# Kernel tuning notes

Hardware: AMD Instinct MI355X
Metric: run time of the kernel (lower is better)

## Reference

```python
import jax, jax.numpy as jnp
import numpy as np
import math

B, S, D, H = 2, 2048, 1024, 16
HD = D // H  # head_dim = 64

def setup_inputs() -> dict:
    key = jax.random.key(0)
    ks = jax.random.split(key, 11)
    def n(k, shape, scale=1.0):
        return jax.random.normal(k, shape, dtype=jnp.float32) * scale
    w_scale = 1.0 / math.sqrt(D)
    return {
        "q": n(ks[0], (B, S, D)),
        "k": n(ks[1], (B, S, D)),
        "v": n(ks[2], (B, S, D)),
        "WQ_w": n(ks[3], (D, D), w_scale),
        "WQ_b": n(ks[4], (D,), 0.01),
        "WK_w": n(ks[5], (D, D), w_scale),
        "WK_b": n(ks[6], (D,), 0.01),
        "WV_w": n(ks[7], (D, D), w_scale),
        "WV_b": n(ks[8], (D,), 0.01),
        "Wout_w": n(ks[9], (D, D), w_scale),
        "Wout_b": n(ks[10], (D,), 0.01),
    }

def reference(q, k, v, WQ_w, WQ_b, WK_w, WK_b, WV_w, WV_b, Wout_w, Wout_b):
    b, s, _ = k.shape
    # QKV projections (torch Linear: x @ W.T + b; here weights stored [in, out])
    qh = (q @ WQ_w + WQ_b).reshape(b, -1, H, HD).transpose(0, 2, 1, 3)  # [b,h,s,hd]
    kh = (k @ WK_w + WK_b).reshape(b, -1, H, HD).transpose(0, 2, 1, 3)
    vh = (v @ WV_w + WV_b).reshape(b, -1, H, HD).transpose(0, 2, 1, 3)
    # naive attention: full [b,h,s,s] score matrix
    scores = jnp.einsum("bhqd,bhkd->bhqk", qh, kh) / math.sqrt(HD)
    attn = jax.nn.softmax(scores, axis=-1)
    out = jnp.einsum("bhqk,bhkd->bhqd", attn, vh)
    concat = out.transpose(0, 2, 1, 3).reshape(b, -1, H * HD)  # [b,s,inner_dim]
    return concat @ Wout_w + Wout_b
```

## Files before the change

### kernel.cpp

```cpp
#include <hip/hip_runtime.h>
#include <hip/hip_bf16.h>
#include <stdint.h>

typedef __attribute__((ext_vector_type(8))) short bf16x8;
typedef __attribute__((ext_vector_type(4))) short short4v;
typedef __attribute__((ext_vector_type(4))) float f32x4;

#define MFMA16x16x32 __builtin_amdgcn_mfma_f32_16x16x32_bf16

__device__ __forceinline__ short f2b(float f) {
  union { float f; uint32_t u; } x;
  x.f = f;
  uint32_t u = x.u;
  uint32_t r = (u + 0x7FFFu + ((u >> 16) & 1u)) >> 16;
  return (short)(uint16_t)r;
}

__device__ __forceinline__ uint32_t cvt_pk_bf16(float lo, float hi) {
  uint32_t r;
  asm volatile("v_cvt_pk_bf16_f32 %0, %1, %2" : "=v"(r) : "v"(lo), "v"(hi));
  return r;
}
__device__ __forceinline__ float exp2_fast(float x) {
  float r;
  asm volatile("v_exp_f32 %0, %1" : "=v"(r) : "v"(x));
  return r;
}
__device__ __forceinline__ bf16x8 cvt8(const float4 a, const float4 b) {
  union { uint32_t u[4]; bf16x8 v; } o;
  o.u[0] = cvt_pk_bf16(a.x, a.y);
  o.u[1] = cvt_pk_bf16(a.z, a.w);
  o.u[2] = cvt_pk_bf16(b.x, b.y);
  o.u[3] = cvt_pk_bf16(b.z, b.w);
  return o.v;
}

__device__ __forceinline__ void async_copy16(const void* g, void* l) {
  __builtin_amdgcn_global_load_lds(
      (const __attribute__((address_space(1))) void*)g,
      (__attribute__((address_space(3))) void*)l, 16, 0, 0);
}

__global__ void prep_kernel(const float* __restrict__ W0,
                            const float* __restrict__ W1,
                            const float* __restrict__ W2,
                            const float* __restrict__ W3,
                            const float* __restrict__ q,
                            const float* __restrict__ k,
                            const float* __restrict__ v,
                            short* __restrict__ Wt,
                            short* __restrict__ xq,
                            short* __restrict__ xk,
                            short* __restrict__ xv) {
  __shared__ short tile[64][72];
  const int z = blockIdx.z;
  const int t = threadIdx.x;
  if (z < 4) {
    const float* W = (z == 0) ? W0 : (z == 1) ? W1 : (z == 2) ? W2 : W3;
    short* Wo = Wt + (size_t)z * 1024 * 1024;
    const int r0 = blockIdx.y * 64;
    const int c0 = blockIdx.x * 64;
#pragma unroll
    for (int i = 0; i < 4; ++i) {
      const int lin = i * 1024 + t * 4;
      const int r = lin >> 6, c = lin & 63;
      const float4 vv = *(const float4*)&W[(size_t)(r0 + r) * 1024 + c0 + c];
      tile[r][c + 0] = f2b(vv.x);
      tile[r][c + 1] = f2b(vv.y);
      tile[r][c + 2] = f2b(vv.z);
      tile[r][c + 3] = f2b(vv.w);
    }
    __syncthreads();
#pragma unroll
    for (int i = 0; i < 2; ++i) {
      const int lin = i * 2048 + t * 8;
      const int r = lin >> 6, c = lin & 63;
      bf16x8 ov;
#pragma unroll
      for (int jj = 0; jj < 8; ++jj) ov[jj] = tile[c + jj][r];
      *(bf16x8*)&Wo[(size_t)(c0 + r) * 1024 + r0 + c] = ov;
    }
  } else {
    const float* x = (z == 4) ? q : (z == 5) ? k : v;
    short* yp = (z == 4) ? xq : (z == 5) ? xk : xv;
    const int base = (blockIdx.y * 16 + blockIdx.x) * 256 + t;
#pragma unroll
    for (int j = 0; j < 8; ++j) {
      const int i = base + j * 65536;
      const float4 a = ((const float4*)x)[2 * i];
      const float4 b = ((const float4*)x)[2 * i + 1];
      ((bf16x8*)yp)[i] = cvt8(a, b);
    }
  }
}

__launch_bounds__(256, 2)
__global__ void gemm_qkv_kernel(const short* __restrict__ A0,
                                const short* __restrict__ A1,
                                const short* __restrict__ A2,
                                const short* __restrict__ WtBase,
                                const float* __restrict__ b0,
                                const float* __restrict__ b1,
                                const float* __restrict__ b2,
                                short* __restrict__ C0,
                                short* __restrict__ C1,
                                short* __restrict__ Vt,
                                int ybase) {
  const int K = 1024;
  __shared__ short As[128 * 64];
  __shared__ short Bs[128 * 64];

  const int y = blockIdx.y + ybase;
  const short* A = (y == 0) ? A0 : (y == 1) ? A1 : A2;
  const short* Wt = WtBase + (size_t)y * 1024 * 1024;
  const float* bias = (y == 0) ? b0 : (y == 1) ? b1 : b2;

  const int tm = blockIdx.x & 31;
  const int tn = blockIdx.x >> 5;
  const int m0 = tm * 128, n0 = tn * 128;

  const int tid = threadIdx.x;
  const int lane = tid & 63;
  const int w = tid >> 6;
  const int wr = w >> 1, wc = w & 1;
  const int hi = lane >> 4, cc = lane & 15;
  const int srow = lane >> 3, schunk = lane & 7;

  f32x4 acc[4][4] = {};

  for (int kt = 0; kt < 16; ++kt) {
    const int k0 = kt * 64;
#pragma unroll
    for (int i = 0; i < 4; ++i) {
      const int ri = w * 4 + i;
      const int row = ri * 8 + srow;
      const int gch = schunk ^ (row & 7);
      async_copy16(A + (size_t)(m0 + row) * K + (k0 + gch * 8), &As[ri * 512]);
      async_copy16(Wt + (size_t)(n0 + row) * K + (k0 + gch * 8), &Bs[ri * 512]);
    }
    __syncthreads();
#pragma unroll
    for (int kk = 0; kk < 2; ++kk) {
      bf16x8 af[4], bfr[4];
#pragma unroll
      for (int x = 0; x < 4; ++x) {
        const int gch = kk * 4 + hi;
        const int rowA = wr * 64 + x * 16 + cc;
        af[x] = *(const bf16x8*)&As[rowA * 64 + ((gch ^ (rowA & 7)) << 3)];
        const int rowB = wc * 64 + x * 16 + cc;
        bfr[x] = *(const bf16x8*)&Bs[rowB * 64 + ((gch ^ (rowB & 7)) << 3)];
      }
#pragma unroll
      for (int x = 0; x < 4; ++x)
#pragma unroll
        for (int yy = 0; yy < 4; ++yy)
          acc[x][yy] = MFMA16x16x32(af[x], bfr[yy], acc[x][yy], 0, 0, 0);
    }
    __syncthreads();
  }

  short* Cout = (y == 0) ? C0 : C1;
#pragma unroll
  for (int x = 0; x < 4; ++x) {
    const int rbase = m0 + wr * 64 + x * 16 + (hi << 2);
#pragma unroll
    for (int yy = 0; yy < 4; ++yy) {
      const int col = n0 + wc * 64 + yy * 16 + cc;
      const float bv = bias[col];
      if (y == 2) {
        const int b = rbase >> 11, s = rbase & 2047;
        const int hh = col >> 6, d = col & 63;
        short4v pack;
#pragma unroll
        for (int r = 0; r < 4; ++r) pack[r] = f2b(acc[x][yy][r] + bv);
        *(short4v*)&Vt[((size_t)(b * 16 + hh) * 64 + d) * 2048 + s] = pack;
      } else {
#pragma unroll
        for (int r = 0; r < 4; ++r)
          Cout[(size_t)(rbase + r) * 1024 + col] = f2b(acc[x][yy][r] + bv);
      }
    }
  }
}

__launch_bounds__(256, 2)
__global__ void gemm_out_kernel(const short* __restrict__ A,
                                const short* __restrict__ Wt,
                                const float* __restrict__ bias,
                                float* __restrict__ C) {
  const int N = 1024, K = 1024;
  __shared__ short As[128 * 64];
  __shared__ short Bs[128 * 64];

  const int tm = blockIdx.x & 31;
  const int tn = blockIdx.x >> 5;
  const int m0 = tm * 128, n0 = tn * 128;

  const int tid = threadIdx.x;
  const int lane = tid & 63;
  const int w = tid >> 6;
  const int wr = w >> 1, wc = w & 1;
  const int hi = lane >> 4, cc = lane & 15;
  const int srow = lane >> 3, schunk = lane & 7;

  f32x4 acc[4][4] = {};

  for (int kt = 0; kt < 16; ++kt) {
    const int k0 = kt * 64;
#pragma unroll
    for (int i = 0; i < 4; ++i) {
      const int ri = w * 4 + i;
      const int row = ri * 8 + srow;
      const int gch = schunk ^ (row & 7);
      async_copy16(A + (size_t)(m0 + row) * K + (k0 + gch * 8), &As[ri * 512]);
      async_copy16(Wt + (size_t)(n0 + row) * K + (k0 + gch * 8), &Bs[ri * 512]);
    }
    __syncthreads();
#pragma unroll
    for (int kk = 0; kk < 2; ++kk) {
      bf16x8 af[4], bfr[4];
#pragma unroll
      for (int x = 0; x < 4; ++x) {
        const int gch = kk * 4 + hi;
        const int rowA = wr * 64 + x * 16 + cc;
        af[x] = *(const bf16x8*)&As[rowA * 64 + ((gch ^ (rowA & 7)) << 3)];
        const int rowB = wc * 64 + x * 16 + cc;
        bfr[x] = *(const bf16x8*)&Bs[rowB * 64 + ((gch ^ (rowB & 7)) << 3)];
      }
#pragma unroll
      for (int x = 0; x < 4; ++x)
#pragma unroll
        for (int yy = 0; yy < 4; ++yy)
          acc[x][yy] = MFMA16x16x32(af[x], bfr[yy], acc[x][yy], 0, 0, 0);
    }
    __syncthreads();
  }

#pragma unroll
  for (int x = 0; x < 4; ++x) {
    const int rbase = m0 + wr * 64 + x * 16 + (hi << 2);
#pragma unroll
    for (int yy = 0; yy < 4; ++yy) {
      const int col = n0 + wc * 64 + yy * 16 + cc;
      const float bv = bias[col];
#pragma unroll
      for (int r = 0; r < 4; ++r)
        C[(size_t)(rbase + r) * N + col] = acc[x][yy][r] + bv;
    }
  }
}

__launch_bounds__(256, 2)
__global__ void attn_kernel(const short* __restrict__ qh,
                            const short* __restrict__ kh,
                            const short* __restrict__ Vt,
                            short* __restrict__ concat) {
  const float CL2 = 0.18033688011112042f;
  __shared__ short Ks[2][64 * 64];
  __shared__ short Vs[2][64 * 64];

  const int qb = blockIdx.x;
  const int h = blockIdx.y;
  const int b = blockIdx.z;
  const int tid = threadIdx.x, lane = tid & 63, w = tid >> 6;
  const int hi = lane >> 4, cc = lane & 15;

  const size_t rowbase = (size_t)b * 2048;
  const int q0 = qb * 128 + w * 32;

  bf16x8 qf[2][2];
#pragma unroll
  for (int aq = 0; aq < 2; ++aq)
#pragma unroll
    for (int kk = 0; kk < 2; ++kk) {
      const int col = h * 64 + kk * 32 + hi * 8;
      qf[aq][kk] =
          *(const bf16x8*)&qh[(rowbase + q0 + aq * 16 + cc) * 1024 + col];
    }

  f32x4 oacc[2][4] = {};
  float l[2] = {0.f, 0.f};
  bf16x8 vf[2][4];
  uint32_t pu[2][4][2];

  const short* Vth = Vt + (size_t)(b * 16 + h) * 64 * 2048;
  const int srow = lane >> 3, schunk = lane & 7;
  const int fKr = (((cc >> 2) & 1) << 2) | (cc & 3);

  auto STAGE = [&](int tile, int buf) {
#pragma unroll
    for (int i = 0; i < 2; ++i) {
      const int ri = w * 2 + i;
      const int row = ri * 8 + srow;
      const int gchK = schunk ^ ((((ri) & 1) << 2) | (srow & 3));
      const int gchV = schunk ^ (row & 7);
      async_copy16(&kh[(rowbase + tile * 64 + row) * 1024 + h * 64 + gchK * 8],
                   &Ks[buf][ri * 512]);
      async_copy16(&Vth[(size_t)row * 2048 + tile * 64 + gchV * 8],
                   &Vs[buf][ri * 512]);
    }
  };
  auto QK = [&](int buf, f32x4 (&sacc)[2][4]) {
#pragma unroll
    for (int kk = 0; kk < 2; ++kk) {
      bf16x8 kf[4];
#pragma unroll
      for (int n = 0; n < 4; ++n) {
        const int row = ((n >> 1) << 5) + (((cc >> 2)) << 3) + ((n & 1) << 2) +
                        (cc & 3);
        const int ch = (kk * 4 + hi) ^ fKr;
        kf[n] = *(const bf16x8*)&Ks[buf][row * 64 + (ch << 3)];
      }
#pragma unroll
      for (int aq = 0; aq < 2; ++aq)
#pragma unroll
        for (int n = 0; n < 4; ++n)
          sacc[aq][n] = MFMA16x16x32(kf[n], qf[aq][kk], sacc[aq][n], 0, 0, 0);
    }
  };
  auto LOADV = [&](int buf) {
#pragma unroll
    for (int kvh = 0; kvh < 2; ++kvh) {
      const int ch = (kvh * 4 + hi) ^ (cc & 7);
#pragma unroll
      for (int n = 0; n < 4; ++n)
        vf[kvh][n] =
            *(const bf16x8*)&Vs[buf][(n * 16 + cc) * 64 + (ch << 3)];
    }
  };
  auto SOFTMAX = [&](f32x4 (&sacc)[2][4]) {
#pragma unroll
    for (int aq = 0; aq < 2; ++aq)
#pragma unroll
      for (int n = 0; n < 4; ++n) {
        const float p0 = exp2_fast(sacc[aq][n][0] * CL2);
        const float p1 = exp2_fast(sacc[aq][n][1] * CL2);
        const float p2 = exp2_fast(sacc[aq][n][2] * CL2);
        const float p3 = exp2_fast(sacc[aq][n][3] * CL2);
        l[aq] += (p0 + p1) + (p2 + p3);
        pu[aq][n][0] = cvt_pk_bf16(p0, p1);
        pu[aq][n][1] = cvt_pk_bf16(p2, p3);
      }
  };
  auto PV = [&]() {
#pragma unroll
    for (int kvh = 0; kvh < 2; ++kvh)
#pragma unroll
      for (int aq = 0; aq < 2; ++aq) {
        union { uint32_t u[4]; bf16x8 v; } pf;
        pf.u[0] = pu[aq][2 * kvh][0];
        pf.u[1] = pu[aq][2 * kvh][1];
        pf.u[2] = pu[aq][2 * kvh + 1][0];
        pf.u[3] = pu[aq][2 * kvh + 1][1];
#pragma unroll
        for (int n = 0; n < 4; ++n)
          oacc[aq][n] = MFMA16x16x32(vf[kvh][n], pf.v, oacc[aq][n], 0, 0, 0);
      }
  };

  STAGE(0, 0);
  __syncthreads();
  {
    STAGE(1, 1);
    f32x4 sacc[2][4] = {};
    QK(0, sacc);
    LOADV(0);
    SOFTMAX(sacc);
    __syncthreads();
  }

  for (int t = 1; t < 32; ++t) {
    const int cur = t & 1;
    if (t + 1 < 32) STAGE(t + 1, cur ^ 1);
    f32x4 sacc[2][4] = {};
    QK(cur, sacc);
    PV();
    LOADV(cur);
    SOFTMAX(sacc);
    __syncthreads();
  }
  PV();

#pragma unroll
  for (int aq = 0; aq < 2; ++aq) {
    float lv = l[aq];
    lv += __shfl_xor(lv, 16);
    lv += __shfl_xor(lv, 32);
    const float inv = 1.0f / lv;
    const size_t grow = rowbase + q0 + aq * 16 + cc;
#pragma unroll
    for (int n = 0; n < 4; ++n)
#pragma unroll
      for (int r = 0; r < 4; ++r) {
        const int d = n * 16 + hi * 4 + r;
        concat[grow * 1024 + h * 64 + d] = f2b(oacc[aq][n][r] * inv);
      }
  }
}

extern "C" void kernel_launch(void* const* d_in, const int* in_sizes, int n_in,
                              void* d_out, int out_size, void* d_ws, size_t ws_size,
                              hipStream_t stream) {
  const float* q = (const float*)d_in[0];
  const float* k = (const float*)d_in[1];
  const float* v = (const float*)d_in[2];
  const float* WQ = (const float*)d_in[3];
  const float* bQ = (const float*)d_in[4];
  const float* WK = (const float*)d_in[5];
  const float* bK = (const float*)d_in[6];
  const float* WV = (const float*)d_in[7];
  const float* bV = (const float*)d_in[8];
  const float* WO = (const float*)d_in[9];
  const float* bO = (const float*)d_in[10];

  char* ws = (char*)d_ws;
  const size_t MB = 1024 * 1024;
  short* Wt = (short*)ws;
  short* xq = (short*)(ws + 8 * MB);
  short* xk = (short*)(ws + 16 * MB);
  short* xv = (short*)(ws + 24 * MB);
  short* qh = (short*)(ws + 32 * MB);
  short* kh = (short*)(ws + 40 * MB);
  short* concat = xk;

  prep_kernel<<<dim3(16, 16, 7), 256, 0, stream>>>(WQ, WK, WV, WO, q, k, v,
                                                   Wt, xq, xk, xv);

  if (ws_size >= 56 * MB) {
    short* Vt = (short*)(ws + 48 * MB);
    gemm_qkv_kernel<<<dim3(256, 3), 256, 0, stream>>>(
        xq, xk, xv, Wt, bQ, bK, bV, qh, kh, Vt, 0);
    attn_kernel<<<dim3(16, 16, 2), 256, 0, stream>>>(qh, kh, Vt, concat);
  } else {
    short* Vt = xq;
    gemm_qkv_kernel<<<dim3(256, 2), 256, 0, stream>>>(
        xq, xk, xv, Wt, bQ, bK, bV, qh, kh, Vt, 0);
    gemm_qkv_kernel<<<dim3(256, 1), 256, 0, stream>>>(
        xq, xk, xv, Wt, bQ, bK, bV, qh, kh, Vt, 2);
    attn_kernel<<<dim3(16, 16, 2), 256, 0, stream>>>(qh, kh, Vt, concat);
  }

  gemm_out_kernel<<<256, 256, 0, stream>>>(concat, Wt + 3 * MB, bO,
                                           (float*)d_out);
}
```

Baseline: 115.8 us.

## Double-buffer GEMM LDS tiles and fold softmax scale into Q projection

```diff
diff --git a/kernel.cpp b/kernel.cpp
--- a/kernel.cpp
+++ b/kernel.cpp
@@ -7,6 +7,7 @@
 typedef __attribute__((ext_vector_type(4))) float f32x4;
 
 #define MFMA16x16x32 __builtin_amdgcn_mfma_f32_16x16x32_bf16
+#define CL2F 0.18033688011112042f
 
 __device__ __forceinline__ short f2b(float f) {
   union { float f; uint32_t u; } x;
@@ -107,8 +108,8 @@
                                 short* __restrict__ Vt,
                                 int ybase) {
   const int K = 1024;
-  __shared__ short As[128 * 64];
-  __shared__ short Bs[128 * 64];
+  __shared__ short As[2][128 * 64];
+  __shared__ short Bs[2][128 * 64];
 
   const int y = blockIdx.y + ybase;
   const short* A = (y == 0) ? A0 : (y == 1) ? A1 : A2;
@@ -128,17 +129,25 @@
 
   f32x4 acc[4][4] = {};
 
-  for (int kt = 0; kt < 16; ++kt) {
+  auto STAGE = [&](int kt, int buf) {
     const int k0 = kt * 64;
 #pragma unroll
     for (int i = 0; i < 4; ++i) {
       const int ri = w * 4 + i;
       const int row = ri * 8 + srow;
       const int gch = schunk ^ (row & 7);
-      async_copy16(A + (size_t)(m0 + row) * K + (k0 + gch * 8), &As[ri * 512]);
-      async_copy16(Wt + (size_t)(n0 + row) * K + (k0 + gch * 8), &Bs[ri * 512]);
-    }
+      async_copy16(A + (size_t)(m0 + row) * K + (k0 + gch * 8),
+                   &As[buf][ri * 512]);
+      async_copy16(Wt + (size_t)(n0 + row) * K + (k0 + gch * 8),
+                   &Bs[buf][ri * 512]);
+    }
+  };
+
+  STAGE(0, 0);
+  for (int kt = 0; kt < 16; ++kt) {
+    const int cur = kt & 1;
     __syncthreads();
+    if (kt < 15) STAGE(kt + 1, cur ^ 1);
 #pragma unroll
     for (int kk = 0; kk < 2; ++kk) {
       bf16x8 af[4], bfr[4];
@@ -146,9 +155,9 @@
       for (int x = 0; x < 4; ++x) {
         const int gch = kk * 4 + hi;
         const int rowA = wr * 64 + x * 16 + cc;
-        af[x] = *(const bf16x8*)&As[rowA * 64 + ((gch ^ (rowA & 7)) << 3)];
+        af[x] = *(const bf16x8*)&As[cur][rowA * 64 + ((gch ^ (rowA & 7)) << 3)];
         const int rowB = wc * 64 + x * 16 + cc;
-        bfr[x] = *(const bf16x8*)&Bs[rowB * 64 + ((gch ^ (rowB & 7)) << 3)];
+        bfr[x] = *(const bf16x8*)&Bs[cur][rowB * 64 + ((gch ^ (rowB & 7)) << 3)];
       }
 #pragma unroll
       for (int x = 0; x < 4; ++x)
@@ -156,7 +165,6 @@
         for (int yy = 0; yy < 4; ++yy)
           acc[x][yy] = MFMA16x16x32(af[x], bfr[yy], acc[x][yy], 0, 0, 0);
     }
-    __syncthreads();
   }
 
   short* Cout = (y == 0) ? C0 : C1;
@@ -176,8 +184,11 @@
         *(short4v*)&Vt[((size_t)(b * 16 + hh) * 64 + d) * 2048 + s] = pack;
       } else {
 #pragma unroll
-        for (int r = 0; r < 4; ++r)
-          Cout[(size_t)(rbase + r) * 1024 + col] = f2b(acc[x][yy][r] + bv);
+        for (int r = 0; r < 4; ++r) {
+          float val = acc[x][yy][r] + bv;
+          if (y == 0) val *= CL2F;
+          Cout[(size_t)(rbase + r) * 1024 + col] = f2b(val);
+        }
       }
     }
   }
@@ -189,8 +200,8 @@
                                 const float* __restrict__ bias,
                                 float* __restrict__ C) {
   const int N = 1024, K = 1024;
-  __shared__ short As[128 * 64];
-  __shared__ short Bs[128 * 64];
+  __shared__ short As[2][128 * 64];
+  __shared__ short Bs[2][128 * 64];
 
   const int tm = blockIdx.x & 31;
   const int tn = blockIdx.x >> 5;
@@ -205,17 +216,25 @@
 
   f32x4 acc[4][4] = {};
 
-  for (int kt = 0; kt < 16; ++kt) {
+  auto STAGE = [&](int kt, int buf) {
     const int k0 = kt * 64;
 #pragma unroll
     for (int i = 0; i < 4; ++i) {
       const int ri = w * 4 + i;
       const int row = ri * 8 + srow;
       const int gch = schunk ^ (row & 7);
-      async_copy16(A + (size_t)(m0 + row) * K + (k0 + gch * 8), &As[ri * 512]);
-      async_copy16(Wt + (size_t)(n0 + row) * K + (k0 + gch * 8), &Bs[ri * 512]);
-    }
+      async_copy16(A + (size_t)(m0 + row) * K + (k0 + gch * 8),
+                   &As[buf][ri * 512]);
+      async_copy16(Wt + (size_t)(n0 + row) * K + (k0 + gch * 8),
+                   &Bs[buf][ri * 512]);
+    }
+  };
+
+  STAGE(0, 0);
+  for (int kt = 0; kt < 16; ++kt) {
+    const int cur = kt & 1;
     __syncthreads();
+    if (kt < 15) STAGE(kt + 1, cur ^ 1);
 #pragma unroll
     for (int kk = 0; kk < 2; ++kk) {
       bf16x8 af[4], bfr[4];
@@ -223,9 +242,9 @@
       for (int x = 0; x < 4; ++x) {
         const int gch = kk * 4 + hi;
         const int rowA = wr * 64 + x * 16 + cc;
-        af[x] = *(const bf16x8*)&As[rowA * 64 + ((gch ^ (rowA & 7)) << 3)];
+        af[x] = *(const bf16x8*)&As[cur][rowA * 64 + ((gch ^ (rowA & 7)) << 3)];
         const int rowB = wc * 64 + x * 16 + cc;
-        bfr[x] = *(const bf16x8*)&Bs[rowB * 64 + ((gch ^ (rowB & 7)) << 3)];
+        bfr[x] = *(const bf16x8*)&Bs[cur][rowB * 64 + ((gch ^ (rowB & 7)) << 3)];
       }
 #pragma unroll
       for (int x = 0; x < 4; ++x)
@@ -233,7 +252,6 @@
         for (int yy = 0; yy < 4; ++yy)
           acc[x][yy] = MFMA16x16x32(af[x], bfr[yy], acc[x][yy], 0, 0, 0);
     }
-    __syncthreads();
   }
 
 #pragma unroll
@@ -255,7 +273,6 @@
                             const short* __restrict__ kh,
                             const short* __restrict__ Vt,
                             short* __restrict__ concat) {
-  const float CL2 = 0.18033688011112042f;
   __shared__ short Ks[2][64 * 64];
   __shared__ short Vs[2][64 * 64];
 
@@ -333,10 +350,10 @@
     for (int aq = 0; aq < 2; ++aq)
 #pragma unroll
       for (int n = 0; n < 4; ++n) {
-        const float p0 = exp2_fast(sacc[aq][n][0] * CL2);
-        const float p1 = exp2_fast(sacc[aq][n][1] * CL2);
-        const float p2 = exp2_fast(sacc[aq][n][2] * CL2);
-        const float p3 = exp2_fast(sacc[aq][n][3] * CL2);
+        const float p0 = exp2_fast(sacc[aq][n][0]);
+        const float p1 = exp2_fast(sacc[aq][n][1]);
+        const float p2 = exp2_fast(sacc[aq][n][2]);
+        const float p3 = exp2_fast(sacc[aq][n][3]);
         l[aq] += (p0 + p1) + (p2 + p3);
         pu[aq][n][0] = cvt_pk_bf16(p0, p1);
         pu[aq][n][1] = cvt_pk_bf16(p2, p3);
```

After: 131.2 us. 13.3% more time.
